# Kernel optimization log

Hardware: AMD Instinct MI355X
Metric: run time of the kernel (lower is better)

Reference implementation:

```python
import jax, jax.numpy as jnp
import numpy as np

T, B, OBS, ACT = 512, 256, 64, 8
H, C = 1024, 512  # h_size, cell_size


def setup_inputs() -> dict:
    key = jax.random.key(0)
    ks = jax.random.split(key, 12)
    u = lambda k, shape, s: jax.random.uniform(k, shape, jnp.float32, -s, s)
    inp = {
        "xs": jax.random.normal(ks[0], (T, B, OBS), jnp.float32),
        "h0": jnp.zeros((B, C), jnp.float32),
        "c0": jnp.zeros((B, C), jnp.float32),
        "h_masks": (jax.random.uniform(ks[1], (T, B, 1)) < 0.05).astype(jnp.float32),
        # input_layer (kaiming-ish uniform fan-in init)
        "W_in": u(ks[2], (H, OBS), 1.0 / np.sqrt(OBS)),
        "b_in": jnp.zeros((H,), jnp.float32),
        # LSTMCell params, PyTorch layout: gates order (i, f, g, o), [4C, in]
        "W_ih": u(ks[3], (4 * C, H), 1.0 / np.sqrt(C)),
        "b_ih": u(ks[4], (4 * C,), 1.0 / np.sqrt(C)),
        "W_hh": u(ks[5], (4 * C, C), 1.0 / np.sqrt(C)),
        "b_hh": u(ks[6], (4 * C,), 1.0 / np.sqrt(C)),
        # mean_layer with mini_weight_init: U(-0.003, 0.003), zero bias
        "W_mean": u(ks[7], (ACT, C), 0.003),
        "b_mean": jnp.zeros((ACT,), jnp.float32),
        "log_std_param": jax.random.normal(ks[8], (ACT,)) * 1e-10 - 1.0,
    }
    return inp


def reference(xs, h0, c0, h_masks, W_in, b_in, W_ih, b_ih, W_hh, b_hh,
              W_mean, b_mean, log_std_param):
    # xs: [T, B, OBS] -> relu embedding [T, B, H]
    x_emb = jax.nn.relu(jnp.einsum('tbo,ho->tbh', xs, W_in) + b_in)
    # Precompute the input-to-gates GEMM for all timesteps at once: [T, B, 4C]
    gx = jnp.einsum('tbh,gh->tbg', x_emb, W_ih) + b_ih

    cell = W_hh.shape[1]

    def step(carry, inp):
        h, c = carry
        g_x, mask = inp                      # g_x: [B,4C], mask: [B,1]
        keep = 1.0 - mask
        h = h * keep
        c = c * keep
        gates = g_x + h @ W_hh.T + b_hh      # [B, 4C]
        i, f, g, o = jnp.split(gates, 4, axis=-1)
        c = jax.nn.sigmoid(f) * c + jax.nn.sigmoid(i) * jnp.tanh(g)
        h = jax.nn.sigmoid(o) * jnp.tanh(c)
        return (h, c), h

    (h_T, c_T), hiddens = jax.lax.scan(step, (h0, c0), (gx, h_masks))
    # hiddens: [T, B, C]
    means = jnp.tanh(jnp.einsum('tbc,ac->tba', hiddens, W_mean) + b_mean)
    log_std = jnp.broadcast_to(log_std_param, means.shape)
    return means, log_std, h_T, c_T
```

## Files before the change

### kernel.cpp

```cpp
#include <hip/hip_runtime.h>
#include <cstdint>
#include <cstddef>

typedef unsigned short ushort_t;
typedef unsigned int uint_t;
typedef __attribute__((ext_vector_type(8))) __bf16 bf16x8;
typedef __attribute__((ext_vector_type(4))) float f32x4;
typedef __attribute__((ext_vector_type(2))) unsigned int u32x2;

static constexpr int T_STEPS = 512;
static constexpr int BATCH   = 256;
static constexpr int OBS_D   = 64;
static constexpr int ACT_D   = 8;
static constexpr int HID_D   = 1024;
static constexpr int CELL_D  = 512;
static constexpr int GATE_D  = 4 * CELL_D;
static constexpr int SCAN_BLOCKS = 256;

__device__ __forceinline__ float bf2f(ushort_t s) {
    uint_t u = ((uint_t)s) << 16;
    float f;
    __builtin_memcpy(&f, &u, 4);
    return f;
}
__device__ __forceinline__ ushort_t f2bf(float x) {
    uint_t u;
    __builtin_memcpy(&u, &x, 4);
    u += 0x7fffu + ((u >> 16) & 1u);
    return (ushort_t)(u >> 16);
}

__device__ __forceinline__ float sigmoid_fast(float x) {
    return __builtin_amdgcn_rcpf(1.f + __expf(-x));
}
__device__ __forceinline__ float tanh_fast(float x) {
    const float e = __expf(-2.f * fabsf(x));
    const float r = (1.f - e) * __builtin_amdgcn_rcpf(1.f + e);
    return copysignf(r, x);
}

__global__ __launch_bounds__(256)
void cvt_f32_bf16(const float* __restrict__ in, ushort_t* __restrict__ out)
{
    const size_t i = ((size_t)blockIdx.x * 256 + threadIdx.x) * 8;
    const float4 v0 = *(const float4*)(in + i);
    const float4 v1 = *(const float4*)(in + i + 4);
    uint4 p;
    p.x = (uint_t)f2bf(v0.x) | ((uint_t)f2bf(v0.y) << 16);
    p.y = (uint_t)f2bf(v0.z) | ((uint_t)f2bf(v0.w) << 16);
    p.z = (uint_t)f2bf(v1.x) | ((uint_t)f2bf(v1.y) << 16);
    p.w = (uint_t)f2bf(v1.z) | ((uint_t)f2bf(v1.w) << 16);
    *(uint4*)(out + i) = p;
}

__global__ __launch_bounds__(256)
void permute_gate_rows(const float* __restrict__ W, ushort_t* __restrict__ Wp, int K)
{
    const int P = blockIdx.x;
    const int c = P >> 2, g = P & 3;
    const float* src = W + (size_t)(g * CELL_D + c) * K;
    ushort_t* dst = Wp + (size_t)P * K;
    for (int k = threadIdx.x; k < K; k += 256) dst[k] = f2bf(src[k]);
}

__global__ __launch_bounds__(256)
void permute_whh_rows(const float* __restrict__ W, ushort_t* __restrict__ Wp, int K)
{
    const int P = blockIdx.x;
    const int blk = P >> 6, rl = P & 63;
    const int t = rl >> 4, qq = (rl >> 2) & 3, r = rl & 3;
    const float* src = W + (size_t)(r * CELL_D + blk * 16 + t * 4 + qq) * K;
    ushort_t* dst = Wp + (size_t)P * K;
    for (int k = threadIdx.x; k < K; k += 256) dst[k] = f2bf(src[k]);
}

__global__ __launch_bounds__(256)
void permute_bias(const float* __restrict__ b, float* __restrict__ bp)
{
    const int P = blockIdx.x * 256 + threadIdx.x;
    bp[P] = b[(P & 3) * CELL_D + (P >> 2)];
}

template<int OUT_MODE>
__global__ __launch_bounds__(256)
void gemm_mfma_nt(const ushort_t* __restrict__ A, const ushort_t* __restrict__ B,
                  const float* __restrict__ bias, void* __restrict__ out_,
                  int N, int K)
{
    __shared__ __align__(16) ushort_t As[128 * 32];
    __shared__ __align__(16) ushort_t Bs[128 * 32];
    const int tid  = threadIdx.x;
    const int lane = tid & 63;
    const int wid  = tid >> 6;
    const int wr   = (wid >> 1) * 64;
    const int wc   = (wid & 1) * 64;
    const int m0 = blockIdx.y * 128;
    const int n0 = blockIdx.x * 128;

    const int srow = tid >> 2;
    const int sv   = tid & 3;
    const int fr   = lane & 15;
    const int fo   = lane >> 4;

    f32x4 acc[4][4];
#pragma unroll
    for (int i = 0; i < 4; ++i)
#pragma unroll
        for (int j = 0; j < 4; ++j) acc[i][j] = (f32x4){0.f, 0.f, 0.f, 0.f};

    const ushort_t* Apt = A + (size_t)(m0 + srow) * K + sv * 8;
    const ushort_t* Bpt = B + (size_t)(n0 + srow) * K + sv * 8;
    uint4* As4 = (uint4*)As;
    uint4* Bs4 = (uint4*)Bs;
    const bf16x8* Af = (const bf16x8*)As;
    const bf16x8* Bf = (const bf16x8*)Bs;

    for (int k0 = 0; k0 < K; k0 += 32) {
        const uint4 a0 = *(const uint4*)(Apt + k0);
        const uint4 a1 = *(const uint4*)(Apt + (size_t)64 * K + k0);
        const uint4 b0 = *(const uint4*)(Bpt + k0);
        const uint4 b1 = *(const uint4*)(Bpt + (size_t)64 * K + k0);
        __syncthreads();
        As4[srow * 4 + sv]        = a0;
        As4[(64 + srow) * 4 + sv] = a1;
        Bs4[srow * 4 + sv]        = b0;
        Bs4[(64 + srow) * 4 + sv] = b1;
        __syncthreads();

        bf16x8 av[4], bv[4];
#pragma unroll
        for (int m = 0; m < 4; ++m) av[m] = Af[(wr + m * 16 + fr) * 4 + fo];
#pragma unroll
        for (int n = 0; n < 4; ++n) bv[n] = Bf[(wc + n * 16 + fr) * 4 + fo];
#pragma unroll
        for (int m = 0; m < 4; ++m)
#pragma unroll
            for (int n = 0; n < 4; ++n)
                acc[m][n] = __builtin_amdgcn_mfma_f32_16x16x32_bf16(
                    av[m], bv[n], acc[m][n], 0, 0, 0);
    }

#pragma unroll
    for (int n = 0; n < 4; ++n) {
        const int col = n0 + wc + n * 16 + fr;
        const float bvv = bias[col];
#pragma unroll
        for (int m = 0; m < 4; ++m) {
            const int row0 = m0 + wr + m * 16 + fo * 4;
#pragma unroll
            for (int r = 0; r < 4; ++r) {
                const float v = acc[m][n][r] + bvv;
                if constexpr (OUT_MODE == 1)
                    ((ushort_t*)out_)[(size_t)(row0 + r) * N + col] = f2bf(fmaxf(v, 0.f));
                else if constexpr (OUT_MODE == 2)
                    ((ushort_t*)out_)[(size_t)(row0 + r) * N + col] = f2bf(v);
                else
                    ((float*)out_)[(size_t)(row0 + r) * N + col] = v;
            }
        }
    }
}

__device__ __forceinline__ void loadq1(uint4 (&d)[4], const ushort_t* hr, int base)
{
#pragma unroll
    for (int j = 0; j < 4; ++j) d[j] = *(const uint4*)(hr + (base + j) * 32);
}

__device__ __forceinline__ void compq1(const uint4 (&d)[4],
                                       const char* wsrow, int q16, int xmask,
                                       int base, f32x4& acc)
{
#pragma unroll
    for (int j = 0; j < 4; ++j) {
        bf16x8 hv;
        __builtin_memcpy(&hv, &d[j], 16);
        const int koff = ((base + j) * 64 + q16) ^ xmask;
        const bf16x8 av = *(const bf16x8*)(wsrow + koff);
        acc = __builtin_amdgcn_mfma_f32_16x16x32_bf16(av, hv, acc, 0, 0, 0);
    }
}

__global__ __launch_bounds__(512)
void lstm_scan(const ushort_t* __restrict__ gx_p,
               const ushort_t* __restrict__ Whh_p,
               const float* __restrict__ b_hh,
               const float* __restrict__ masks_c,
               const ushort_t* h_init,
               float* __restrict__ c_state,
               ushort_t* hid,
               float* __restrict__ hT_f32,
               int Tc, int is_last,
               uint_t* __restrict__ bar)
{
    __shared__ __align__(16) ushort_t Ws[64 * 512];

    const int tid  = threadIdx.x;
    const int lane = tid & 63;
    const int w8   = tid >> 6;
    const int w    = w8 & 3;
    const int nfl  = w8 >> 2;
    const int q    = lane >> 4;
    const int s    = lane & 15;
    const int x    = blockIdx.x & 7;
    const int j    = blockIdx.x >> 3;
    const int xmask = (s & 7) << 4;
    const int q16  = q * 16;
    const int cell = j * 16 + w * 4 + q;

    for (int idx = tid; idx < 64 * 64; idx += 512) {
        const int row = idx >> 6;
        const int c16 = idx & 63;
        const uint4 v = *(const uint4*)(Whh_p + (size_t)(j * 64 + row) * CELL_D + c16 * 8);
        *(uint4*)((char*)Ws + row * 1024 + ((c16 * 16) ^ ((row & 7) << 4))) = v;
    }

    const int b = x * 32 + nfl * 16 + s;

    float creg = c_state[(size_t)b * CELL_D + cell];
    float bh[4];
#pragma unroll
    for (int r = 0; r < 4; ++r) bh[r] = b_hh[r * CELL_D + cell];

    float mv;
    uint2 gxv;
    auto prefetch_step = [&](int TL) {
        gxv = *(const uint2*)(gx_p + ((size_t)TL * BATCH + b) * GATE_D + cell * 4);
        mv  = masks_c[(size_t)TL * BATCH + b];
    };

    const char* wsrow = (const char*)Ws + (w * 16 + s) * 1024;
    __syncthreads();

    for (int tl = 0; tl < Tc; ++tl) {
        const ushort_t* hp = (tl == 0) ? h_init
                                       : hid + (size_t)(tl - 1) * BATCH * CELL_D;
        const ushort_t* hr = hp + (size_t)b * CELL_D + q * 8;

        uint64_t ready = 0;
        const uint_t tgt_in = (uint_t)tl;
        auto waitg = [&](int g) {
            const uint64_t need = 0xFFull << (g * 8);
            if ((ready & need) != need) {
                const uint_t* fp = bar + x * 32 + (lane & 31);
                for (;;) {
                    uint_t v;
                    asm volatile("global_load_dword %0, %1, off sc0 sc1\n\t"
                                 "s_waitcnt vmcnt(0)"
                                 : "=v"(v) : "v"(fp) : "memory");
                    ready = __ballot((int)(v >= tgt_in)) & 0xFFFFFFFFull;
                    if ((ready & need) == need) break;
                    __builtin_amdgcn_s_sleep(1);
                }
            }
            asm volatile("" ::: "memory");
        };

        f32x4 acc = (f32x4){0.f, 0.f, 0.f, 0.f};

        uint4 A[4], B[4];
        if (tl) waitg(0);
        loadq1(A, hr, 0);
        prefetch_step(tl);
        if (tl) waitg(1);
        loadq1(B, hr, 4);
        compq1(A, wsrow, q16, xmask, 0, acc);
        if (tl) waitg(2);
        loadq1(A, hr, 8);
        compq1(B, wsrow, q16, xmask, 4, acc);
        if (tl) waitg(3);
        loadq1(B, hr, 12);
        compq1(A, wsrow, q16, xmask, 8, acc);
        compq1(B, wsrow, q16, xmask, 12, acc);

        const float keep = (mv > 0.5f) ? 0.f : 1.f;
        const ushort_t* gp = (const ushort_t*)&gxv;
        const float gi = fmaf(acc[0], keep, bf2f(gp[0]) + bh[0]);
        const float gf = fmaf(acc[1], keep, bf2f(gp[1]) + bh[1]);
        const float gg = fmaf(acc[2], keep, bf2f(gp[2]) + bh[2]);
        const float go = fmaf(acc[3], keep, bf2f(gp[3]) + bh[3]);
        const float cn = sigmoid_fast(gf) * (creg * keep)
                       + sigmoid_fast(gi) * tanh_fast(gg);
        const float hn = sigmoid_fast(go) * tanh_fast(cn);
        creg = cn;

        const uint_t hv = (uint_t)f2bf(hn);
        const uint_t vA = (uint_t)__shfl((int)hv, s + 16);
        const uint_t vB = (uint_t)__shfl((int)hv, s + 32);
        const uint_t vC = (uint_t)__shfl((int)hv, s + 48);
        if (q == 0) {
            u32x2 r0;
            r0[0] = hv | (vA << 16);
            r0[1] = vB | (vC << 16);
            ushort_t* d0 = hid + (size_t)tl * BATCH * CELL_D
                         + (size_t)b * CELL_D + j * 16 + w * 4;
            asm volatile("global_store_dwordx2 %0, %1, off sc0 sc1"
                         :: "v"(d0), "v"(r0) : "memory");
        }
        if (is_last && tl == Tc - 1)
            hT_f32[(size_t)b * CELL_D + cell] = hn;

        if (tl == Tc - 1) break;

        asm volatile("s_waitcnt vmcnt(0)" ::: "memory");
        __builtin_amdgcn_s_barrier();
        if (tid == 0) {
            const uint_t tgt = (uint_t)(tl + 1);
            asm volatile("global_store_dword %0, %1, off sc0 sc1"
                         :: "v"(bar + x * 32 + j), "v"(tgt) : "memory");
        }
    }

    c_state[(size_t)b * CELL_D + cell] = creg;
}

__global__ __launch_bounds__(256)
void mean_head(const ushort_t* __restrict__ hiddens, const float* __restrict__ W_mean,
               const float* __restrict__ b_mean, const float* __restrict__ log_std,
               float* __restrict__ means_out, float* __restrict__ logstd_out)
{
    __shared__ float Wm[8][516];
    const int tid = threadIdx.x;
#pragma unroll
    for (int i = 0; i < 16; ++i) {
        int idx = i * 256 + tid;
        Wm[idx >> 9][idx & 511] = W_mean[idx];
    }
    __syncthreads();
    const int r = tid >> 3, a = tid & 7;
    const size_t m = (size_t)blockIdx.x * 32 + r;
    const ushort_t* hp = hiddens + m * CELL_D;
    float acc = 0.f;
#pragma unroll 2
    for (int k8 = 0; k8 < 64; ++k8) {
        const uint4 v = *(const uint4*)(hp + k8 * 8);
        const ushort_t* pv = (const ushort_t*)&v;
        const float* wv = &Wm[a][k8 * 8];
#pragma unroll
        for (int e = 0; e < 8; ++e) acc = fmaf(bf2f(pv[e]), wv[e], acc);
    }
    means_out[m * ACT_D + a]  = tanhf(acc + b_mean[a]);
    logstd_out[m * ACT_D + a] = log_std[a];
}

extern "C" void kernel_launch(void* const* d_in, const int* in_sizes, int n_in,
                              void* d_out, int out_size, void* d_ws, size_t ws_size,
                              hipStream_t stream)
{
    const float* xs     = (const float*)d_in[0];
    const float* h0     = (const float*)d_in[1];
    const float* c0     = (const float*)d_in[2];
    const float* masks  = (const float*)d_in[3];
    const float* W_in   = (const float*)d_in[4];
    const float* b_in   = (const float*)d_in[5];
    const float* W_ih   = (const float*)d_in[6];
    const float* b_ih   = (const float*)d_in[7];
    const float* W_hh   = (const float*)d_in[8];
    const float* b_hh   = (const float*)d_in[9];
    const float* W_mean = (const float*)d_in[10];
    const float* b_mean = (const float*)d_in[11];
    const float* lstd   = (const float*)d_in[12];

    const int M = T_STEPS * BATCH;
    const size_t stateB = (size_t)BATCH * CELL_D * sizeof(float);

    const size_t szWhh  = (size_t)GATE_D * CELL_D * 2;
    const size_t szWih  = (size_t)GATE_D * HID_D * 2;
    const size_t szWin  = (size_t)HID_D * OBS_D * 2;
    const size_t szH0b  = (size_t)BATCH * CELL_D * 2;
    const size_t szBih  = (size_t)GATE_D * 4;
    const size_t szBar  = 1024;
    const size_t fixed  = szWhh + szWih + szWin + szH0b + szBih + szBar + stateB;

    const size_t per_tc = (size_t)BATCH * GATE_D * 2
                        + (size_t)BATCH * CELL_D * 2
                        + (size_t)BATCH * HID_D * 2
                        + (size_t)BATCH * OBS_D * 2;
    int Tc = T_STEPS;
    while (Tc > 2 && fixed + per_tc * (size_t)Tc > ws_size) Tc >>= 1;

    char* p = (char*)d_ws;
    ushort_t* Whh_p = (ushort_t*)p;              p += szWhh;
    ushort_t* Wih_p = (ushort_t*)p;              p += szWih;
    ushort_t* Win_b = (ushort_t*)p;              p += szWin;
    ushort_t* h0b   = (ushort_t*)p;              p += szH0b;
    float*    bihp  = (float*)p;                 p += szBih;
    uint_t*   bar   = (uint_t*)p;                p += szBar;
    float*    c_state = (float*)p;               p += stateB;
    ushort_t* gx_p  = (ushort_t*)p;              p += (size_t)Tc * BATCH * GATE_D * 2;
    ushort_t* hid   = (ushort_t*)p;              p += (size_t)Tc * BATCH * CELL_D * 2;
    ushort_t* E     = (ushort_t*)p;              p += (size_t)Tc * BATCH * HID_D * 2;
    ushort_t* xs_b  = (ushort_t*)p;

    float* means_out  = (float*)d_out;
    float* logstd_out = means_out + (size_t)M * ACT_D;
    float* hT_out     = logstd_out + (size_t)M * ACT_D;
    float* cT_out     = hT_out + (size_t)BATCH * CELL_D;

    permute_whh_rows<<<GATE_D, 256, 0, stream>>>(W_hh, Whh_p, CELL_D);
    permute_gate_rows<<<GATE_D, 256, 0, stream>>>(W_ih, Wih_p, HID_D);
    cvt_f32_bf16<<<(HID_D * OBS_D) / 2048, 256, 0, stream>>>(W_in, Win_b);
    cvt_f32_bf16<<<(BATCH * CELL_D) / 2048, 256, 0, stream>>>(h0, h0b);
    permute_bias<<<GATE_D / 256, 256, 0, stream>>>(b_ih, bihp);
    hipMemcpyAsync(c_state, c0, stateB, hipMemcpyDeviceToDevice, stream);

    const int chunks = T_STEPS / Tc;
    for (int ci = 0; ci < chunks; ++ci) {
        const int t0 = ci * Tc;
        const int Mc = Tc * BATCH;

        cvt_f32_bf16<<<(Mc * OBS_D) / 2048, 256, 0, stream>>>(
            xs + (size_t)t0 * BATCH * OBS_D, xs_b);

        gemm_mfma_nt<1><<<dim3(HID_D / 128, Mc / 128), 256, 0, stream>>>(
            xs_b, Win_b, b_in, E, HID_D, OBS_D);

        gemm_mfma_nt<2><<<dim3(GATE_D / 128, Mc / 128), 256, 0, stream>>>(
            E, Wih_p, bihp, gx_p, GATE_D, HID_D);

        hipMemsetAsync(bar, 0, 1024, stream);
        const ushort_t* h_init = (ci == 0) ? h0b
                               : hid + (size_t)(Tc - 1) * BATCH * CELL_D;
        lstm_scan<<<SCAN_BLOCKS, 512, 0, stream>>>(
            gx_p, Whh_p, b_hh, masks + (size_t)t0 * BATCH, h_init,
            c_state, hid, hT_out, Tc, (ci == chunks - 1) ? 1 : 0, bar);

        mean_head<<<Mc / 32, 256, 0, stream>>>(
            hid, W_mean, b_mean, lstd,
            means_out + (size_t)t0 * BATCH * ACT_D,
            logstd_out + (size_t)t0 * BATCH * ACT_D);
    }

    hipMemcpyAsync(cT_out, c_state, stateB, hipMemcpyDeviceToDevice, stream);
}
```

Baseline: 3.726 ms.

## Overlap next-chunk input GEMM and previous mean head with the LSTM scan

Fuses the recurrent scan with extra worker blocks in one launch. The scan blocks run the sequential recurrence at raised priority while the extra blocks compute the next chunk's input-to-gates GEMM and the previous chunk's mean head. gx and hidden buffers are double-buffered, and the time axis is split into chunks of at most 128 steps. The aim is to hide the big gx GEMM and the mean head behind the latency-bound scan. The risk is that worker blocks compete with the scan for CUs, memory bandwidth and L2, which could slow the critical recurrence. Spinning scan blocks also rely on all 256 being co-resident.

```diff
diff --git a/kernel.cpp b/kernel.cpp
--- a/kernel.cpp
+++ b/kernel.cpp
@@ -16,6 +16,7 @@
 static constexpr int CELL_D  = 512;
 static constexpr int GATE_D  = 4 * CELL_D;
 static constexpr int SCAN_BLOCKS = 256;
+static constexpr int WORK_BLOCKS = 256;
 
 __device__ __forceinline__ float bf2f(ushort_t s) {
     uint_t u = ((uint_t)s) << 16;
@@ -181,137 +182,259 @@
     }
 }
 
-__global__ __launch_bounds__(512)
-void lstm_scan(const ushort_t* __restrict__ gx_p,
-               const ushort_t* __restrict__ Whh_p,
-               const float* __restrict__ b_hh,
-               const float* __restrict__ masks_c,
-               const ushort_t* h_init,
-               float* __restrict__ c_state,
-               ushort_t* hid,
-               float* __restrict__ hT_f32,
-               int Tc, int is_last,
-               uint_t* __restrict__ bar)
-{
-    __shared__ __align__(16) ushort_t Ws[64 * 512];
-
+__device__ void gemm_tile_512(const ushort_t* __restrict__ A,
+                              const ushort_t* __restrict__ B,
+                              const float* __restrict__ bias,
+                              ushort_t* __restrict__ out,
+                              int N, int K, int m0, int n0, char* sh)
+{
+    uint4* As4 = (uint4*)sh;
+    uint4* Bs4 = (uint4*)(sh + 8192);
+    const bf16x8* Af = (const bf16x8*)sh;
+    const bf16x8* Bf = (const bf16x8*)(sh + 8192);
     const int tid  = threadIdx.x;
     const int lane = tid & 63;
-    const int w8   = tid >> 6;
-    const int w    = w8 & 3;
-    const int nfl  = w8 >> 2;
-    const int q    = lane >> 4;
-    const int s    = lane & 15;
-    const int x    = blockIdx.x & 7;
-    const int j    = blockIdx.x >> 3;
-    const int xmask = (s & 7) << 4;
-    const int q16  = q * 16;
-    const int cell = j * 16 + w * 4 + q;
-
-    for (int idx = tid; idx < 64 * 64; idx += 512) {
-        const int row = idx >> 6;
-        const int c16 = idx & 63;
-        const uint4 v = *(const uint4*)(Whh_p + (size_t)(j * 64 + row) * CELL_D + c16 * 8);
-        *(uint4*)((char*)Ws + row * 1024 + ((c16 * 16) ^ ((row & 7) << 4))) = v;
-    }
-
-    const int b = x * 32 + nfl * 16 + s;
-
-    float creg = c_state[(size_t)b * CELL_D + cell];
-    float bh[4];
-#pragma unroll
-    for (int r = 0; r < 4; ++r) bh[r] = b_hh[r * CELL_D + cell];
-
-    float mv;
-    uint2 gxv;
-    auto prefetch_step = [&](int TL) {
-        gxv = *(const uint2*)(gx_p + ((size_t)TL * BATCH + b) * GATE_D + cell * 4);
-        mv  = masks_c[(size_t)TL * BATCH + b];
-    };
-
-    const char* wsrow = (const char*)Ws + (w * 16 + s) * 1024;
-    __syncthreads();
-
-    for (int tl = 0; tl < Tc; ++tl) {
-        const ushort_t* hp = (tl == 0) ? h_init
-                                       : hid + (size_t)(tl - 1) * BATCH * CELL_D;
-        const ushort_t* hr = hp + (size_t)b * CELL_D + q * 8;
-
-        uint64_t ready = 0;
-        const uint_t tgt_in = (uint_t)tl;
-        auto waitg = [&](int g) {
-            const uint64_t need = 0xFFull << (g * 8);
-            if ((ready & need) != need) {
-                const uint_t* fp = bar + x * 32 + (lane & 31);
-                for (;;) {
-                    uint_t v;
-                    asm volatile("global_load_dword %0, %1, off sc0 sc1\n\t"
-                                 "s_waitcnt vmcnt(0)"
-                                 : "=v"(v) : "v"(fp) : "memory");
-                    ready = __ballot((int)(v >= tgt_in)) & 0xFFFFFFFFull;
-                    if ((ready & need) == need) break;
-                    __builtin_amdgcn_s_sleep(1);
+    const int wid  = tid >> 6;
+    const int wr   = (wid & 3) * 32;
+    const int wc   = (wid >> 2) * 64;
+    const int srow = tid >> 2;
+    const int sv   = tid & 3;
+    const int fr   = lane & 15;
+    const int fo   = lane >> 4;
+
+    f32x4 acc[2][4];
+#pragma unroll
+    for (int m = 0; m < 2; ++m)
+#pragma unroll
+        for (int n = 0; n < 4; ++n) acc[m][n] = (f32x4){0.f, 0.f, 0.f, 0.f};
+
+    const ushort_t* Apt = A + (size_t)(m0 + srow) * K + sv * 8;
+    const ushort_t* Bpt = B + (size_t)(n0 + srow) * K + sv * 8;
+
+    for (int k0 = 0; k0 < K; k0 += 32) {
+        const uint4 a0 = *(const uint4*)(Apt + k0);
+        const uint4 b0 = *(const uint4*)(Bpt + k0);
+        __syncthreads();
+        As4[srow * 4 + sv] = a0;
+        Bs4[srow * 4 + sv] = b0;
+        __syncthreads();
+
+        bf16x8 av[2], bv[4];
+#pragma unroll
+        for (int m = 0; m < 2; ++m) av[m] = Af[(wr + m * 16 + fr) * 4 + fo];
+#pragma unroll
+        for (int n = 0; n < 4; ++n) bv[n] = Bf[(wc + n * 16 + fr) * 4 + fo];
+#pragma unroll
+        for (int m = 0; m < 2; ++m)
+#pragma unroll
+            for (int n = 0; n < 4; ++n)
+                acc[m][n] = __builtin_amdgcn_mfma_f32_16x16x32_bf16(
+                    av[m], bv[n], acc[m][n], 0, 0, 0);
+    }
+
+#pragma unroll
+    for (int n = 0; n < 4; ++n) {
+        const int col = n0 + wc + n * 16 + fr;
+        const float bvv = bias[col];
+#pragma unroll
+        for (int m = 0; m < 2; ++m) {
+            const int row0 = m0 + wr + m * 16 + fo * 4;
+#pragma unroll
+            for (int r = 0; r < 4; ++r)
+                out[(size_t)(row0 + r) * N + col] = f2bf(acc[m][n][r] + bvv);
+        }
+    }
+}
+
+__global__ __launch_bounds__(512, 4)
+void fused_scan(const ushort_t* __restrict__ gx_p,
+                const ushort_t* __restrict__ Whh_p,
+                const float* __restrict__ b_hh,
+                const float* __restrict__ masks_c,
+                const ushort_t* h_init,
+                float* __restrict__ c_state,
+                ushort_t* __restrict__ hid,
+                float* __restrict__ hT_f32,
+                int Tc, int is_last,
+                uint_t* __restrict__ bar,
+                int do_gemm,
+                const ushort_t* __restrict__ E,
+                const ushort_t* __restrict__ Wih_p,
+                const float* __restrict__ bihp,
+                ushort_t* __restrict__ gx_next,
+                int do_mean,
+                const ushort_t* __restrict__ hid_prev,
+                const float* __restrict__ W_mean,
+                const float* __restrict__ b_mean,
+                const float* __restrict__ lstd,
+                float* __restrict__ means_prev,
+                float* __restrict__ logstd_prev)
+{
+    __shared__ __align__(16) char shmem[64 * 1024];
+
+    if (blockIdx.x < SCAN_BLOCKS) {
+        __builtin_amdgcn_s_setprio(1);
+        ushort_t* Ws = (ushort_t*)shmem;
+
+        const int tid  = threadIdx.x;
+        const int lane = tid & 63;
+        const int w8   = tid >> 6;
+        const int w    = w8 & 3;
+        const int nfl  = w8 >> 2;
+        const int q    = lane >> 4;
+        const int s    = lane & 15;
+        const int x    = blockIdx.x & 7;
+        const int j    = blockIdx.x >> 3;
+        const int xmask = (s & 7) << 4;
+        const int q16  = q * 16;
+        const int cell = j * 16 + w * 4 + q;
+
+        for (int idx = tid; idx < 64 * 64; idx += 512) {
+            const int row = idx >> 6;
+            const int c16 = idx & 63;
+            const uint4 v = *(const uint4*)(Whh_p + (size_t)(j * 64 + row) * CELL_D + c16 * 8);
+            *(uint4*)((char*)Ws + row * 1024 + ((c16 * 16) ^ ((row & 7) << 4))) = v;
+        }
+
+        const int b = x * 32 + nfl * 16 + s;
+
+        float creg = c_state[(size_t)b * CELL_D + cell];
+        float bh[4];
+#pragma unroll
+        for (int r = 0; r < 4; ++r) bh[r] = b_hh[r * CELL_D + cell];
+
+        float mv;
+        uint2 gxv;
+        auto prefetch_step = [&](int TL) {
+            gxv = *(const uint2*)(gx_p + ((size_t)TL * BATCH + b) * GATE_D + cell * 4);
+            mv  = masks_c[(size_t)TL * BATCH + b];
+        };
+
+        const char* wsrow = (const char*)Ws + (w * 16 + s) * 1024;
+        __syncthreads();
+
+        for (int tl = 0; tl < Tc; ++tl) {
+            const ushort_t* hp = (tl == 0) ? h_init
+                                           : hid + (size_t)(tl - 1) * BATCH * CELL_D;
+            const ushort_t* hr = hp + (size_t)b * CELL_D + q * 8;
+
+            uint64_t ready = 0;
+            const uint_t tgt_in = (uint_t)tl;
+            auto waitg = [&](int g) {
+                const uint64_t need = 0xFFull << (g * 8);
+                if ((ready & need) != need) {
+                    const uint_t* fp = bar + x * 32 + (lane & 31);
+                    for (;;) {
+                        uint_t v;
+                        asm volatile("global_load_dword %0, %1, off sc0 sc1\n\t"
+                                     "s_waitcnt vmcnt(0)"
+                                     : "=v"(v) : "v"(fp) : "memory");
+                        ready = __ballot((int)(v >= tgt_in)) & 0xFFFFFFFFull;
+                        if ((ready & need) == need) break;
+                        __builtin_amdgcn_s_sleep(1);
+                    }
                 }
+                asm volatile("" ::: "memory");
+            };
+
+            f32x4 acc = (f32x4){0.f, 0.f, 0.f, 0.f};
+
+            uint4 A[4], B[4];
+            if (tl) waitg(0);
+            loadq1(A, hr, 0);
+            prefetch_step(tl);
+            if (tl) waitg(1);
+            loadq1(B, hr, 4);
+            compq1(A, wsrow, q16, xmask, 0, acc);
+            if (tl) waitg(2);
+            loadq1(A, hr, 8);
+            compq1(B, wsrow, q16, xmask, 4, acc);
+            if (tl) waitg(3);
+            loadq1(B, hr, 12);
+            compq1(A, wsrow, q16, xmask, 8, acc);
+            compq1(B, wsrow, q16, xmask, 12, acc);
+
+            const float keep = (mv > 0.5f) ? 0.f : 1.f;
+            const ushort_t* gp = (const ushort_t*)&gxv;
+            const float gi = fmaf(acc[0], keep, bf2f(gp[0]) + bh[0]);
+            const float gf = fmaf(acc[1], keep, bf2f(gp[1]) + bh[1]);
+            const float gg = fmaf(acc[2], keep, bf2f(gp[2]) + bh[2]);
+            const float go = fmaf(acc[3], keep, bf2f(gp[3]) + bh[3]);
+            const float cn = sigmoid_fast(gf) * (creg * keep)
+                           + sigmoid_fast(gi) * tanh_fast(gg);
+            const float hn = sigmoid_fast(go) * tanh_fast(cn);
+            creg = cn;
+
+            const uint_t hv = (uint_t)f2bf(hn);
+            const uint_t vA = (uint_t)__shfl((int)hv, s + 16);
+            const uint_t vB = (uint_t)__shfl((int)hv, s + 32);
+            const uint_t vC = (uint_t)__shfl((int)hv, s + 48);
+            if (q == 0) {
+                u32x2 r0;
+                r0[0] = hv | (vA << 16);
+                r0[1] = vB | (vC << 16);
+                ushort_t* d0 = hid + (size_t)tl * BATCH * CELL_D
+                             + (size_t)b * CELL_D + j * 16 + w * 4;
+                asm volatile("global_store_dwordx2 %0, %1, off sc0 sc1"
+                             :: "v"(d0), "v"(r0) : "memory");
             }
-            asm volatile("" ::: "memory");
-        };
-
-        f32x4 acc = (f32x4){0.f, 0.f, 0.f, 0.f};
-
-        uint4 A[4], B[4];
-        if (tl) waitg(0);
-        loadq1(A, hr, 0);
-        prefetch_step(tl);
-        if (tl) waitg(1);
-        loadq1(B, hr, 4);
-        compq1(A, wsrow, q16, xmask, 0, acc);
-        if (tl) waitg(2);
-        loadq1(A, hr, 8);
-        compq1(B, wsrow, q16, xmask, 4, acc);
-        if (tl) waitg(3);
-        loadq1(B, hr, 12);
-        compq1(A, wsrow, q16, xmask, 8, acc);
-        compq1(B, wsrow, q16, xmask, 12, acc);
-
-        const float keep = (mv > 0.5f) ? 0.f : 1.f;
-        const ushort_t* gp = (const ushort_t*)&gxv;
-        const float gi = fmaf(acc[0], keep, bf2f(gp[0]) + bh[0]);
-        const float gf = fmaf(acc[1], keep, bf2f(gp[1]) + bh[1]);
-        const float gg = fmaf(acc[2], keep, bf2f(gp[2]) + bh[2]);
-        const float go = fmaf(acc[3], keep, bf2f(gp[3]) + bh[3]);
-        const float cn = sigmoid_fast(gf) * (creg * keep)
-                       + sigmoid_fast(gi) * tanh_fast(gg);
-        const float hn = sigmoid_fast(go) * tanh_fast(cn);
-        creg = cn;
-
-        const uint_t hv = (uint_t)f2bf(hn);
-        const uint_t vA = (uint_t)__shfl((int)hv, s + 16);
-        const uint_t vB = (uint_t)__shfl((int)hv, s + 32);
-        const uint_t vC = (uint_t)__shfl((int)hv, s + 48);
-        if (q == 0) {
-            u32x2 r0;
-            r0[0] = hv | (vA << 16);
-            r0[1] = vB | (vC << 16);
-            ushort_t* d0 = hid + (size_t)tl * BATCH * CELL_D
-                         + (size_t)b * CELL_D + j * 16 + w * 4;
-            asm volatile("global_store_dwordx2 %0, %1, off sc0 sc1"
-                         :: "v"(d0), "v"(r0) : "memory");
+            if (is_last && tl == Tc - 1)
+                hT_f32[(size_t)b * CELL_D + cell] = hn;
+
+            if (tl == Tc - 1) break;
+
+            asm volatile("s_waitcnt vmcnt(0)" ::: "memory");
+            __builtin_amdgcn_s_barrier();
+            if (tid == 0) {
+                const uint_t tgt = (uint_t)(tl + 1);
+                asm volatile("global_store_dword %0, %1, off sc0 sc1"
+                             :: "v"(bar + x * 32 + j), "v"(tgt) : "memory");
+            }
         }
-        if (is_last && tl == Tc - 1)
-            hT_f32[(size_t)b * CELL_D + cell] = hn;
-
-        if (tl == Tc - 1) break;
-
-        asm volatile("s_waitcnt vmcnt(0)" ::: "memory");
-        __builtin_amdgcn_s_barrier();
-        if (tid == 0) {
-            const uint_t tgt = (uint_t)(tl + 1);
-            asm volatile("global_store_dword %0, %1, off sc0 sc1"
-                         :: "v"(bar + x * 32 + j), "v"(tgt) : "memory");
+
+        c_state[(size_t)b * CELL_D + cell] = creg;
+    } else {
+        const int wbid = blockIdx.x - SCAN_BLOCKS;
+        const int tid  = threadIdx.x;
+
+        if (do_gemm) {
+            const int mtiles = (Tc * BATCH) / 128;
+            const int tiles  = mtiles * (GATE_D / 128);
+            for (int t = wbid; t < tiles; t += WORK_BLOCKS) {
+                const int m0 = (t >> 4) * 128;
+                const int n0 = (t & 15) * 128;
+                gemm_tile_512(E, Wih_p, bihp, gx_next, GATE_D, HID_D, m0, n0, shmem);
+            }
         }
-    }
-
-    c_state[(size_t)b * CELL_D + cell] = creg;
+
+        if (do_mean) {
+            __syncthreads();
+            float (*Wm)[516] = (float(*)[516])shmem;
+#pragma unroll
+            for (int i = 0; i < 8; ++i) {
+                int idx = i * 512 + tid;
+                Wm[idx >> 9][idx & 511] = W_mean[idx];
+            }
+            __syncthreads();
+            const int r = tid >> 3, a = tid & 7;
+            const int units = (Tc * BATCH) / 64;
+            for (int u = wbid; u < units; u += WORK_BLOCKS) {
+                const size_t m = (size_t)u * 64 + r;
+                const ushort_t* hp = hid_prev + m * CELL_D;
+                float acc = 0.f;
+#pragma unroll 2
+                for (int k8 = 0; k8 < 64; ++k8) {
+                    const uint4 v = *(const uint4*)(hp + k8 * 8);
+                    const ushort_t* pv = (const ushort_t*)&v;
+                    const float* wv = &Wm[a][k8 * 8];
+#pragma unroll
+                    for (int e = 0; e < 8; ++e) acc = fmaf(bf2f(pv[e]), wv[e], acc);
+                }
+                means_prev[m * ACT_D + a]  = tanhf(acc + b_mean[a]);
+                logstd_prev[m * ACT_D + a] = lstd[a];
+            }
+        }
+    }
 }
 
 __global__ __launch_bounds__(256)
@@ -370,14 +493,17 @@
     const size_t szH0b  = (size_t)BATCH * CELL_D * 2;
     const size_t szBih  = (size_t)GATE_D * 4;
     const size_t szBar  = 1024;
-    const size_t fixed  = szWhh + szWih + szWin + szH0b + szBih + szBar + stateB;
-
-    const size_t per_tc = (size_t)BATCH * GATE_D * 2
-                        + (size_t)BATCH * CELL_D * 2
-                        + (size_t)BATCH * HID_D * 2
-                        + (size_t)BATCH * OBS_D * 2;
-    int Tc = T_STEPS;
-    while (Tc > 2 && fixed + per_tc * (size_t)Tc > ws_size) Tc >>= 1;
+    const size_t szXsb  = (size_t)T_STEPS * BATCH * OBS_D * 2;
+    const size_t fixed  = szWhh + szWih + szWin + szH0b + szBih + szBar + stateB + szXsb;
+
+    const size_t gxStep  = (size_t)BATCH * GATE_D * 2;
+    const size_t hidStep = (size_t)BATCH * CELL_D * 2;
+    const size_t eStep   = (size_t)BATCH * HID_D * 2;
+    const size_t per_tc  = 2 * gxStep + 2 * hidStep + eStep;
+    int Tc = 128;
+    while (Tc > 4 && fixed + per_tc * (size_t)Tc > ws_size) Tc >>= 1;
+    const int chunks = T_STEPS / Tc;
+    const int Mc = Tc * BATCH;
 
     char* p = (char*)d_ws;
     ushort_t* Whh_p = (ushort_t*)p;              p += szWhh;
@@ -387,10 +513,14 @@
     float*    bihp  = (float*)p;                 p += szBih;
     uint_t*   bar   = (uint_t*)p;                p += szBar;
     float*    c_state = (float*)p;               p += stateB;
-    ushort_t* gx_p  = (ushort_t*)p;              p += (size_t)Tc * BATCH * GATE_D * 2;
-    ushort_t* hid   = (ushort_t*)p;              p += (size_t)Tc * BATCH * CELL_D * 2;
-    ushort_t* E     = (ushort_t*)p;              p += (size_t)Tc * BATCH * HID_D * 2;
-    ushort_t* xs_b  = (ushort_t*)p;
+    ushort_t* xs_b  = (ushort_t*)p;              p += szXsb;
+    ushort_t* E     = (ushort_t*)p;              p += eStep * (size_t)Tc;
+    ushort_t* gx0   = (ushort_t*)p;              p += gxStep * (size_t)Tc;
+    ushort_t* gx1   = (ushort_t*)p;              p += gxStep * (size_t)Tc;
+    ushort_t* hid0  = (ushort_t*)p;              p += hidStep * (size_t)Tc;
+    ushort_t* hid1  = (ushort_t*)p;
+    ushort_t* gxb[2]  = {gx0, gx1};
+    ushort_t* hidb[2] = {hid0, hid1};
 
     float* means_out  = (float*)d_out;
     float* logstd_out = means_out + (size_t)M * ACT_D;
@@ -404,32 +534,39 @@
     permute_bias<<<GATE_D / 256, 256, 0, stream>>>(b_ih, bihp);
     hipMemcpyAsync(c_state, c0, stateB, hipMemcpyDeviceToDevice, stream);
 
-    const int chunks = T_STEPS / Tc;
+    cvt_f32_bf16<<<(T_STEPS * BATCH * OBS_D) / 2048, 256, 0, stream>>>(xs, xs_b);
+
+    gemm_mfma_nt<1><<<dim3(HID_D / 128, Mc / 128), 256, 0, stream>>>(
+        xs_b, Win_b, b_in, E, HID_D, OBS_D);
+    gemm_mfma_nt<2><<<dim3(GATE_D / 128, Mc / 128), 256, 0, stream>>>(
+        E, Wih_p, bihp, gxb[0], GATE_D, HID_D);
+
     for (int ci = 0; ci < chunks; ++ci) {
         const int t0 = ci * Tc;
-        const int Mc = Tc * BATCH;
-
-        cvt_f32_bf16<<<(Mc * OBS_D) / 2048, 256, 0, stream>>>(
-            xs + (size_t)t0 * BATCH * OBS_D, xs_b);
-
-        gemm_mfma_nt<1><<<dim3(HID_D / 128, Mc / 128), 256, 0, stream>>>(
-            xs_b, Win_b, b_in, E, HID_D, OBS_D);
-
-        gemm_mfma_nt<2><<<dim3(GATE_D / 128, Mc / 128), 256, 0, stream>>>(
-            E, Wih_p, bihp, gx_p, GATE_D, HID_D);
+        const int do_gemm = (ci + 1 < chunks);
+        const int do_mean = (ci > 0);
+
+        if (do_gemm)
+            gemm_mfma_nt<1><<<dim3(HID_D / 128, Mc / 128), 256, 0, stream>>>(
+                xs_b + (size_t)(t0 + Tc) * BATCH * OBS_D, Win_b, b_in, E, HID_D, OBS_D);
 
         hipMemsetAsync(bar, 0, 1024, stream);
         const ushort_t* h_init = (ci == 0) ? h0b
-                               : hid + (size_t)(Tc - 1) * BATCH * CELL_D;
-        lstm_scan<<<SCAN_BLOCKS, 512, 0, stream>>>(
-            gx_p, Whh_p, b_hh, masks + (size_t)t0 * BATCH, h_init,
-            c_state, hid, hT_out, Tc, (ci == chunks - 1) ? 1 : 0, bar);
-
-        mean_head<<<Mc / 32, 256, 0, stream>>>(
-            hid, W_mean, b_mean, lstd,
-            means_out + (size_t)t0 * BATCH * ACT_D,
-            logstd_out + (size_t)t0 * BATCH * ACT_D);
-    }
+                               : hidb[(ci - 1) & 1] + (size_t)(Tc - 1) * BATCH * CELL_D;
+        const int tp = (ci - 1) * Tc;
+        fused_scan<<<SCAN_BLOCKS + WORK_BLOCKS, 512, 0, stream>>>(
+            gxb[ci & 1], Whh_p, b_hh, masks + (size_t)t0 * BATCH, h_init,
+            c_state, hidb[ci & 1], hT_out, Tc, (ci == chunks - 1) ? 1 : 0, bar,
+            do_gemm, E, Wih_p, bihp, gxb[(ci + 1) & 1],
+            do_mean, hidb[(ci - 1) & 1], W_mean, b_mean, lstd,
+            means_out + (size_t)(do_mean ? tp : 0) * BATCH * ACT_D,
+            logstd_out + (size_t)(do_mean ? tp : 0) * BATCH * ACT_D);
+    }
+
+    mean_head<<<Mc / 32, 256, 0, stream>>>(
+        hidb[(chunks - 1) & 1], W_mean, b_mean, lstd,
+        means_out + (size_t)(chunks - 1) * Tc * BATCH * ACT_D,
+        logstd_out + (size_t)(chunks - 1) * Tc * BATCH * ACT_D);
 
     hipMemcpyAsync(cT_out, c_state, stateB, hipMemcpyDeviceToDevice, stream);
 }
```

Result: slower. 4.682 ms (+25.7%).
